# Kernel optimization log

Measured on AMD Instinct MI355X. Metric: run time of the kernel, lower is better.

## Reference

```python
import jax, jax.numpy as jnp
import numpy as np

EPS = 1e-5


def _conv(x, w, padding, groups=1):
    return jax.lax.conv_general_dilated(
        x, w, window_strides=(1, 1),
        padding=[(padding, padding), (padding, padding)],
        dimension_numbers=("NCHW", "OIHW", "NCHW"),
        feature_group_count=groups)


def _bn(x, gamma, beta, mean, var):
    # inference-mode BatchNorm2d, params shape [C]
    inv = gamma * jax.lax.rsqrt(var + EPS)
    return x * inv[None, :, None, None] + (beta - mean * inv)[None, :, None, None]


def _adder_dw(x, w):
    # depthwise AdderNet 'conv': out[b, c*R+r, h, w] = -sum_{kh,kw} |x[b,c,h+kh-p,w+kw-p] - w[c,r,kh,kw]|
    # x: [B,C,H,W], w: [C,R,K,K] (groups=C, R outputs per group)
    B, C, H, W = x.shape
    R, K = w.shape[1], w.shape[-1]
    p = K // 2
    xp = jnp.pad(x, ((0, 0), (0, 0), (p, p), (p, p)))
    acc = jnp.zeros((B, C, R, H, W), x.dtype)
    for kh in range(K):          # fixed small 3x3 tap loop
        for kw in range(K):
            shift = xp[:, :, kh:kh + H, kw:kw + W]          # [B,C,H,W]
            tap = w[:, :, kh, kw]                           # [C,R]
            acc = acc + jnp.abs(shift[:, :, None] - tap[None, :, :, None, None])
    return -acc.reshape(B, C * R, H, W)


def setup_inputs() -> dict:
    key = jax.random.key(0)
    ks = jax.random.split(key, 12)
    B, Cin, H, W = 32, 240, 56, 56
    init_c, ratio = 24, 10
    r1 = ratio - 1            # 9 ghost channels per primary channel
    new_c = init_c * r1       # 216
    f32 = jnp.float32
    x = jax.random.normal(ks[0], (B, Cin, H, W), f32)
    w_primary = jax.random.normal(ks[1], (init_c, Cin, 1, 1), f32) * 0.05
    w_dw = jax.random.normal(ks[2], (init_c, 1, 3, 3), f32) * 0.1
    w_add = jax.random.normal(ks[3], (init_c, r1, 3, 3), f32) * 0.1
    def bn(kk, c):
        k1, k2 = jax.random.split(kk)
        return (jnp.ones((c,), f32), jnp.zeros((c,), f32),
                jax.random.normal(k1, (c,), f32) * 0.1,
                jax.random.uniform(k2, (c,), f32, 0.5, 1.5))
    g1, b1, m1, v1 = bn(ks[4], init_c)
    g2, b2, m2, v2 = bn(ks[5], init_c)
    g3, b3, m3, v3 = bn(ks[6], new_c)
    return dict(x=x, w_primary=w_primary, g1=g1, b1=b1, m1=m1, v1=v1,
                w_dw=w_dw, g2=g2, b2=b2, m2=m2, v2=v2,
                w_add=w_add, g3=g3, b3=b3, m3=m3, v3=v3)


def reference(x, w_primary, g1, b1, m1, v1, w_dw, g2, b2, m2, v2,
              w_add, g3, b3, m3, v3):
    oup = 240
    init_c = w_primary.shape[0]
    # primary_conv: 1x1 conv -> BN -> depthwise 3x3 conv -> BN -> Identity (relu slot is Identity)
    x1 = _conv(x, w_primary, padding=0)
    x1 = _bn(x1, g1, b1, m1, v1)
    x1 = _conv(x1, w_dw, padding=1, groups=init_c)
    x1 = _bn(x1, g2, b2, m2, v2)
    # cheap_operation: depthwise Adder2D -> BN -> ReLU
    x2 = _adder_dw(x1, w_add)
    x2 = jax.nn.relu(_bn(x2, g3, b3, m3, v3))
    out = jnp.concatenate([x1, x2], axis=1)
    return out[:, :oup]
```

## Files before the change

### kernel.cpp

```cpp
#include <hip/hip_runtime.h>

#define EPS_ 1e-5f
#define BATCH 32
#define CIN 240
#define H_ 56
#define W_ 56
#define HW 3136
#define C1 24
#define R_ 9
#define C2 216
#define COUT 240

#define WS_WT   0
#define WS_B1   5760
#define WS_WDW  5784
#define WS_B2   6000
#define WS_INV3 6024
#define WS_T3   6240
#define WS_T1   8192
#define WS_T1_FLOATS (8192 + BATCH * C1 * HW)

__global__ __launch_bounds__(256) void prep_kernel(
    const float* __restrict__ wp,
    const float* __restrict__ g1, const float* __restrict__ b1,
    const float* __restrict__ m1, const float* __restrict__ v1,
    const float* __restrict__ wdw,
    const float* __restrict__ g2, const float* __restrict__ b2,
    const float* __restrict__ m2, const float* __restrict__ v2,
    const float* __restrict__ g3, const float* __restrict__ b3,
    const float* __restrict__ m3, const float* __restrict__ v3,
    float* __restrict__ ws) {
  int i = blockIdx.x * 256 + threadIdx.x;
  if (i < 5760) {
    int ci = i / C1, co = i % C1;
    float s = g1[co] / sqrtf(v1[co] + EPS_);
    ws[WS_WT + ci * C1 + co] = wp[co * CIN + ci] * s;
    if (ci == 0) ws[WS_B1 + co] = b1[co] - m1[co] * s;
  } else if (i < 5760 + C2) {
    int j = i - 5760;
    int c = j / 9;
    float s = g2[c] / sqrtf(v2[c] + EPS_);
    ws[WS_WDW + j] = wdw[j] * s;
    if (j % 9 == 0) ws[WS_B2 + c] = b2[c] - m2[c] * s;
  } else if (i < 5976 + C2) {
    int j = i - 5976;
    float s = g3[j] / sqrtf(v3[j] + EPS_);
    ws[WS_INV3 + j] = s;
    ws[WS_T3 + j] = b3[j] - m3[j] * s;
  }
}

__global__ __launch_bounds__(256) void conv1x1_kernel(
    const float* __restrict__ x, const float* __restrict__ wt,
    const float* __restrict__ bias1, float* __restrict__ t1b,
    const int cs, const int coff) {
  __shared__ float smem[12288];
  const int tid  = threadIdx.x;
  const int lane = tid & 63;
  const int kq   = tid >> 6;

  for (int i = tid; i < 5760; i += 256) smem[i] = wt[i];
  __syncthreads();

  const int P   = blockIdx.x * 128 + lane * 2;
  const int b   = P / HW;
  const int hw  = P - b * HW;
  const int ci0 = kq * 60;
  const float* xp    = x + ((size_t)b * CIN + ci0) * HW + hw;
  const float* wbase = smem + ci0 * C1;

  float acc[C1][2];
#pragma unroll
  for (int i = 0; i < C1; ++i) { acc[i][0] = 0.f; acc[i][1] = 0.f; }

  float2 A[6], B[6];
#pragma unroll
  for (int j = 0; j < 6; ++j) A[j] = *(const float2*)(xp + (size_t)j * HW);
#pragma unroll
  for (int j = 0; j < 6; ++j) B[j] = *(const float2*)(xp + (size_t)(6 + j) * HW);

  auto consume = [&](const float2* buf, int cb) {
#pragma unroll
    for (int j = 0; j < 6; ++j) {
      const float2 xv = buf[j];
      const float* wr = wbase + (cb + j) * C1;
#pragma unroll
      for (int k = 0; k < 6; ++k) {
        const float4 wq = *(const float4*)(wr + 4 * k);
        acc[4*k+0][0] = fmaf(wq.x, xv.x, acc[4*k+0][0]);
        acc[4*k+0][1] = fmaf(wq.x, xv.y, acc[4*k+0][1]);
        acc[4*k+1][0] = fmaf(wq.y, xv.x, acc[4*k+1][0]);
        acc[4*k+1][1] = fmaf(wq.y, xv.y, acc[4*k+1][1]);
        acc[4*k+2][0] = fmaf(wq.z, xv.x, acc[4*k+2][0]);
        acc[4*k+2][1] = fmaf(wq.z, xv.y, acc[4*k+2][1]);
        acc[4*k+3][0] = fmaf(wq.w, xv.x, acc[4*k+3][0]);
        acc[4*k+3][1] = fmaf(wq.w, xv.y, acc[4*k+3][1]);
      }
    }
  };

#pragma unroll 1
  for (int g = 0; g < 4; ++g) {
    const int c = 12 * g;
    consume(A, c);
#pragma unroll
    for (int j = 0; j < 6; ++j) A[j] = *(const float2*)(xp + (size_t)(c + 12 + j) * HW);
    consume(B, c + 6);
#pragma unroll
    for (int j = 0; j < 6; ++j) B[j] = *(const float2*)(xp + (size_t)(c + 18 + j) * HW);
  }
  consume(A, 48);
  consume(B, 54);
  __syncthreads();

#pragma unroll
  for (int i = 0; i < C1; ++i)
    *(float2*)&smem[(kq * C1 + i) * 128 + 2 * lane] = make_float2(acc[i][0], acc[i][1]);
  __syncthreads();

  float* o = t1b + ((size_t)b * cs + coff) * HW + hw;
#pragma unroll
  for (int i = 0; i < 6; ++i) {
    const int co = kq * 6 + i;
    const float2 p0 = *(const float2*)&smem[(0 * C1 + co) * 128 + 2 * lane];
    const float2 p1 = *(const float2*)&smem[(1 * C1 + co) * 128 + 2 * lane];
    const float2 p2 = *(const float2*)&smem[(2 * C1 + co) * 128 + 2 * lane];
    const float2 p3 = *(const float2*)&smem[(3 * C1 + co) * 128 + 2 * lane];
    const float bsv = bias1[co];
    float2 v;
    v.x = p0.x + p1.x + p2.x + p3.x + bsv;
    v.y = p0.y + p1.y + p2.y + p3.y + bsv;
    *(float2*)(o + (size_t)co * HW) = v;
  }
}

__global__ __launch_bounds__(256) void dwadd_kernel(
    const float* __restrict__ t1b, const float* __restrict__ wdwf,
    const float* __restrict__ bias2, const float* __restrict__ wadd,
    const float* __restrict__ inv3, const float* __restrict__ t3,
    float* __restrict__ out) {
  const int c = blockIdx.y, b = blockIdx.z;
  const int h0 = blockIdx.x * 14;
  __shared__ __align__(16) float t1s[18 * 56];
  __shared__ __align__(16) float x1s[16 * 56];
  __shared__ float taps[R_][3][4];
  __shared__ float s3[R_], t3s[R_];
  const int tid = threadIdx.x;

  const float* t1 = t1b + ((size_t)b * C1 + c) * HW;
  if (tid < 252) {
    const int r  = tid / 14;
    const int w0 = (tid - r * 14) * 4;
    const int gh = h0 - 2 + r;
    float4 v = {0.f, 0.f, 0.f, 0.f};
    if (gh >= 0 && gh < H_) v = *(const float4*)(t1 + gh * W_ + w0);
    *(float4*)&t1s[r * 56 + w0] = v;
  }
  if (tid < 108) {
    int r = tid / 12, kh = (tid / 4) % 3, kw = tid & 3;
    taps[r][kh][kw] = (kw < 3) ? wadd[((c * R_ + r) * 3 + kh) * 3 + kw] : 0.f;
  } else if (tid >= 128 && tid < 128 + R_) {
    int r = tid - 128;
    s3[r]  = inv3[c * R_ + r];
    t3s[r] = t3[c * R_ + r];
  }
  float wk[9];
#pragma unroll
  for (int k = 0; k < 9; ++k) wk[k] = wdwf[c * 9 + k];
  const float bb = bias2[c];
  __syncthreads();

  if (tid < 224) {
    const int r  = tid / 14;
    const int w0 = (tid - r * 14) * 4;
    const int gr = h0 - 1 + r;
    float4 v = {bb, bb, bb, bb};
#pragma unroll
    for (int kh = 0; kh < 3; ++kh) {
      const float* rp = &t1s[(r + kh) * 56];
      const float  l  = (w0 > 0) ? rp[w0 - 1] : 0.f;
      const float4 m  = *(const float4*)(rp + w0);
      const float  rt = (w0 < 52) ? rp[w0 + 4] : 0.f;
      const float t0 = wk[kh * 3 + 0], t1w = wk[kh * 3 + 1], t2 = wk[kh * 3 + 2];
      v.x = fmaf(l,   t0, v.x); v.x = fmaf(m.x, t1w, v.x); v.x = fmaf(m.y, t2, v.x);
      v.y = fmaf(m.x, t0, v.y); v.y = fmaf(m.y, t1w, v.y); v.y = fmaf(m.z, t2, v.y);
      v.z = fmaf(m.y, t0, v.z); v.z = fmaf(m.z, t1w, v.z); v.z = fmaf(m.w, t2, v.z);
      v.w = fmaf(m.z, t0, v.w); v.w = fmaf(m.w, t1w, v.w); v.w = fmaf(rt,  t2, v.w);
    }
    float4 xv = v;
    if (gr < 0 || gr >= H_) { xv.x = 0.f; xv.y = 0.f; xv.z = 0.f; xv.w = 0.f; }
    *(float4*)&x1s[r * 56 + w0] = xv;
    if (r >= 1 && r < 15)
      *(float4*)(out + ((size_t)b * COUT + c) * HW + gr * W_ + w0) = v;
  }
  __syncthreads();

  if (tid < 196) {
    const int r  = tid / 14;
    const int w0 = (tid - r * 14) * 4;
    const int gr = h0 + r;
    float xr[3][6];
#pragma unroll
    for (int kh = 0; kh < 3; ++kh) {
      const float* rp = &x1s[(r + kh) * 56];
      xr[kh][0] = (w0 > 0) ? rp[w0 - 1] : 0.f;
      const float4 m = *(const float4*)(rp + w0);
      xr[kh][1] = m.x; xr[kh][2] = m.y; xr[kh][3] = m.z; xr[kh][4] = m.w;
      xr[kh][5] = (w0 < 52) ? rp[w0 + 4] : 0.f;
    }
    float* ob = out + ((size_t)b * COUT + C1 + c * R_) * HW + gr * W_ + w0;
#pragma unroll
    for (int rr = 0; rr < R_; ++rr) {
      float a0 = 0.f, a1 = 0.f, a2 = 0.f, a3 = 0.f;
#pragma unroll
      for (int kh = 0; kh < 3; ++kh) {
#pragma unroll
        for (int kw = 0; kw < 3; ++kw) {
          const float t = taps[rr][kh][kw];
          a0 += fabsf(xr[kh][kw + 0] - t);
          a1 += fabsf(xr[kh][kw + 1] - t);
          a2 += fabsf(xr[kh][kw + 2] - t);
          a3 += fabsf(xr[kh][kw + 3] - t);
        }
      }
      const float s = s3[rr], tb = t3s[rr];
      float4 v;
      v.x = fmaxf(fmaf(-s, a0, tb), 0.f);
      v.y = fmaxf(fmaf(-s, a1, tb), 0.f);
      v.z = fmaxf(fmaf(-s, a2, tb), 0.f);
      v.w = fmaxf(fmaf(-s, a3, tb), 0.f);
      *(float4*)(ob + (size_t)rr * HW) = v;
    }
  }
}


__global__ __launch_bounds__(256) void dw_kernel(
    const float* __restrict__ outr, const float* __restrict__ wdwf,
    const float* __restrict__ bias2, float* __restrict__ out) {
  const int c = blockIdx.y, b = blockIdx.z;
  const int q = blockIdx.x * 256 + threadIdx.x;
  if (q >= 784) return;
  const int h  = q / 14;
  const int w0 = (q - h * 14) * 4;
  const float* in = outr + ((size_t)b * COUT + C1 + c) * HW;

  float wk[9];
#pragma unroll
  for (int k = 0; k < 9; ++k) wk[k] = wdwf[c * 9 + k];
  const float bb = bias2[c];

  float xr[3][6];
#pragma unroll
  for (int kh = 0; kh < 3; ++kh) {
    const int hh = h + kh - 1;
    const bool rok = (hh >= 0) & (hh < H_);
    const float* rp = in + hh * W_;
    xr[kh][0] = (rok && w0 > 0) ? rp[w0 - 1] : 0.f;
    if (rok) {
      const float4 m = *(const float4*)(rp + w0);
      xr[kh][1] = m.x; xr[kh][2] = m.y; xr[kh][3] = m.z; xr[kh][4] = m.w;
    } else {
      xr[kh][1] = 0.f; xr[kh][2] = 0.f; xr[kh][3] = 0.f; xr[kh][4] = 0.f;
    }
    xr[kh][5] = (rok && w0 < W_ - 4) ? rp[w0 + 4] : 0.f;
  }

  float4 v = {bb, bb, bb, bb};
#pragma unroll
  for (int kh = 0; kh < 3; ++kh) {
#pragma unroll
    for (int kw = 0; kw < 3; ++kw) {
      const float t = wk[kh * 3 + kw];
      v.x = fmaf(xr[kh][kw + 0], t, v.x);
      v.y = fmaf(xr[kh][kw + 1], t, v.y);
      v.z = fmaf(xr[kh][kw + 2], t, v.z);
      v.w = fmaf(xr[kh][kw + 3], t, v.w);
    }
  }
  *(float4*)(out + ((size_t)b * COUT + c) * HW + h * W_ + w0) = v;
}

__global__ __launch_bounds__(256) void adder_kernel(
    const float* __restrict__ outr, const float* __restrict__ wadd,
    const float* __restrict__ inv3, const float* __restrict__ t3,
    float* __restrict__ out) {
  const int c = blockIdx.y, b = blockIdx.z;
  __shared__ float taps[R_][3][4];
  __shared__ float s3[R_], t3s[R_];
  const int tid = threadIdx.x;
  if (tid < 108) {
    int r = tid / 12, kh = (tid / 4) % 3, kw = tid & 3;
    taps[r][kh][kw] = (kw < 3) ? wadd[((c * R_ + r) * 3 + kh) * 3 + kw] : 0.f;
  } else if (tid >= 128 && tid < 128 + R_) {
    int r = tid - 128;
    s3[r]  = inv3[c * R_ + r];
    t3s[r] = t3[c * R_ + r];
  }
  __syncthreads();

  const int q = blockIdx.x * 256 + tid;
  if (q >= 784) return;
  const int h  = q / 14;
  const int w0 = (q - h * 14) * 4;
  const float* in = outr + ((size_t)b * COUT + c) * HW;

  float xr[3][6];
#pragma unroll
  for (int kh = 0; kh < 3; ++kh) {
    const int hh = h + kh - 1;
    const bool rok = (hh >= 0) & (hh < H_);
    const float* rp = in + hh * W_;
    xr[kh][0] = (rok && w0 > 0) ? rp[w0 - 1] : 0.f;
    if (rok) {
      const float4 m = *(const float4*)(rp + w0);
      xr[kh][1] = m.x; xr[kh][2] = m.y; xr[kh][3] = m.z; xr[kh][4] = m.w;
    } else {
      xr[kh][1] = 0.f; xr[kh][2] = 0.f; xr[kh][3] = 0.f; xr[kh][4] = 0.f;
    }
    xr[kh][5] = (rok && w0 < W_ - 4) ? rp[w0 + 4] : 0.f;
  }

#pragma unroll
  for (int r = 0; r < R_; ++r) {
    float a0 = 0.f, a1 = 0.f, a2 = 0.f, a3 = 0.f;
#pragma unroll
    for (int kh = 0; kh < 3; ++kh) {
#pragma unroll
      for (int kw = 0; kw < 3; ++kw) {
        const float t = taps[r][kh][kw];
        a0 += fabsf(xr[kh][kw + 0] - t);
        a1 += fabsf(xr[kh][kw + 1] - t);
        a2 += fabsf(xr[kh][kw + 2] - t);
        a3 += fabsf(xr[kh][kw + 3] - t);
      }
    }
    const float s = s3[r], bb = t3s[r];
    float4 v;
    v.x = fmaxf(fmaf(-s, a0, bb), 0.f);
    v.y = fmaxf(fmaf(-s, a1, bb), 0.f);
    v.z = fmaxf(fmaf(-s, a2, bb), 0.f);
    v.w = fmaxf(fmaf(-s, a3, bb), 0.f);
    *(float4*)(out + ((size_t)b * COUT + C1 + c * R_ + r) * HW + h * W_ + w0) = v;
  }
}

extern "C" void kernel_launch(void* const* d_in, const int* in_sizes, int n_in,
                              void* d_out, int out_size, void* d_ws, size_t ws_size,
                              hipStream_t stream) {
  const float* x    = (const float*)d_in[0];
  const float* wp   = (const float*)d_in[1];
  const float* g1   = (const float*)d_in[2];
  const float* b1   = (const float*)d_in[3];
  const float* m1   = (const float*)d_in[4];
  const float* v1   = (const float*)d_in[5];
  const float* wdw  = (const float*)d_in[6];
  const float* g2   = (const float*)d_in[7];
  const float* b2   = (const float*)d_in[8];
  const float* m2   = (const float*)d_in[9];
  const float* v2   = (const float*)d_in[10];
  const float* wadd = (const float*)d_in[11];
  const float* g3   = (const float*)d_in[12];
  const float* b3   = (const float*)d_in[13];
  const float* m3   = (const float*)d_in[14];
  const float* v3   = (const float*)d_in[15];

  float* ws  = (float*)d_ws;
  float* out = (float*)d_out;

  const bool fused = ws_size >= (size_t)WS_T1_FLOATS * sizeof(float);
  float* t1b;
  int cs, coff;
  if (fused) { t1b = ws + WS_T1; cs = C1;   coff = 0; }
  else       { t1b = out;        cs = COUT; coff = C1; }

  prep_kernel<<<25, 256, 0, stream>>>(wp, g1, b1, m1, v1, wdw, g2, b2, m2, v2,
                                      g3, b3, m3, v3, ws);

  conv1x1_kernel<<<784, 256, 0, stream>>>(x, ws + WS_WT, ws + WS_B1,
                                          t1b, cs, coff);

  if (fused) {
    dwadd_kernel<<<dim3(4, C1, BATCH), 256, 0, stream>>>(
        t1b, ws + WS_WDW, ws + WS_B2, wadd, ws + WS_INV3, ws + WS_T3, out);
  } else {
    dw_kernel<<<dim3(4, C1, BATCH), 256, 0, stream>>>(out, ws + WS_WDW,
                                                      ws + WS_B2, out);
    adder_kernel<<<dim3(4, C1, BATCH), 256, 0, stream>>>(out, wadd,
                                                         ws + WS_INV3,
                                                         ws + WS_T3, out);
  }
}
```

Before: 219.1 us.

## Split conv1x1 output channels across 512 threads and read weights from global

The 1x1 conv kernel now launches 512 threads per block, with each wave group owning 12 of the 24 output channels for one quarter of the input channels. This halves the per-thread accumulator registers. Weights are read straight from global/L1 instead of being staged in LDS, which removes the preload loop and one barrier. The shared-memory reduction is reorganised to match, and an indexing fix offsets the adder kernel's input by C1 channels in the non-fused path.

```diff
diff --git a/kernel.cpp b/kernel.cpp
--- a/kernel.cpp
+++ b/kernel.cpp
@@ -50,28 +50,27 @@
   }
 }
 
-__global__ __launch_bounds__(256) void conv1x1_kernel(
+__global__ __launch_bounds__(512, 6) void conv1x1_kernel(
     const float* __restrict__ x, const float* __restrict__ wt,
     const float* __restrict__ bias1, float* __restrict__ t1b,
     const int cs, const int coff) {
-  __shared__ float smem[12288];
+  __shared__ float red[4 * C1 * 128];
   const int tid  = threadIdx.x;
   const int lane = tid & 63;
   const int kq   = tid >> 6;
-
-  for (int i = tid; i < 5760; i += 256) smem[i] = wt[i];
-  __syncthreads();
+  const int c4   = kq & 3;
+  const int co0  = (kq >> 2) * 12;
 
   const int P   = blockIdx.x * 128 + lane * 2;
   const int b   = P / HW;
   const int hw  = P - b * HW;
-  const int ci0 = kq * 60;
-  const float* xp    = x + ((size_t)b * CIN + ci0) * HW + hw;
-  const float* wbase = smem + ci0 * C1;
-
-  float acc[C1][2];
-#pragma unroll
-  for (int i = 0; i < C1; ++i) { acc[i][0] = 0.f; acc[i][1] = 0.f; }
+  const int ci0 = c4 * 60;
+  const float* xp = x  + ((size_t)b * CIN + ci0) * HW + hw;
+  const float* wb = wt + ci0 * C1 + co0;
+
+  float acc[12][2];
+#pragma unroll
+  for (int i = 0; i < 12; ++i) { acc[i][0] = 0.f; acc[i][1] = 0.f; }
 
   float2 A[6], B[6];
 #pragma unroll
@@ -83,9 +82,9 @@
 #pragma unroll
     for (int j = 0; j < 6; ++j) {
       const float2 xv = buf[j];
-      const float* wr = wbase + (cb + j) * C1;
-#pragma unroll
-      for (int k = 0; k < 6; ++k) {
+      const float* wr = wb + (cb + j) * C1;
+#pragma unroll
+      for (int k = 0; k < 3; ++k) {
         const float4 wq = *(const float4*)(wr + 4 * k);
         acc[4*k+0][0] = fmaf(wq.x, xv.x, acc[4*k+0][0]);
         acc[4*k+0][1] = fmaf(wq.x, xv.y, acc[4*k+0][1]);
@@ -111,21 +110,21 @@
   }
   consume(A, 48);
   consume(B, 54);
+
+#pragma unroll
+  for (int i = 0; i < 12; ++i)
+    *(float2*)&red[(c4 * C1 + co0 + i) * 128 + 2 * lane] =
+        make_float2(acc[i][0], acc[i][1]);
   __syncthreads();
 
-#pragma unroll
-  for (int i = 0; i < C1; ++i)
-    *(float2*)&smem[(kq * C1 + i) * 128 + 2 * lane] = make_float2(acc[i][0], acc[i][1]);
-  __syncthreads();
-
   float* o = t1b + ((size_t)b * cs + coff) * HW + hw;
 #pragma unroll
-  for (int i = 0; i < 6; ++i) {
-    const int co = kq * 6 + i;
-    const float2 p0 = *(const float2*)&smem[(0 * C1 + co) * 128 + 2 * lane];
-    const float2 p1 = *(const float2*)&smem[(1 * C1 + co) * 128 + 2 * lane];
-    const float2 p2 = *(const float2*)&smem[(2 * C1 + co) * 128 + 2 * lane];
-    const float2 p3 = *(const float2*)&smem[(3 * C1 + co) * 128 + 2 * lane];
+  for (int i = 0; i < 3; ++i) {
+    const int co = kq * 3 + i;
+    const float2 p0 = *(const float2*)&red[(0 * C1 + co) * 128 + 2 * lane];
+    const float2 p1 = *(const float2*)&red[(1 * C1 + co) * 128 + 2 * lane];
+    const float2 p2 = *(const float2*)&red[(2 * C1 + co) * 128 + 2 * lane];
+    const float2 p3 = *(const float2*)&red[(3 * C1 + co) * 128 + 2 * lane];
     const float bsv = bias1[co];
     float2 v;
     v.x = p0.x + p1.x + p2.x + p3.x + bsv;
@@ -303,7 +302,7 @@
   if (q >= 784) return;
   const int h  = q / 14;
   const int w0 = (q - h * 14) * 4;
-  const float* in = outr + ((size_t)b * COUT + c) * HW;
+  const float* in = outr + ((size_t)b * COUT + C1 + c) * HW;
 
   float xr[3][6];
 #pragma unroll
@@ -377,7 +376,7 @@
   prep_kernel<<<25, 256, 0, stream>>>(wp, g1, b1, m1, v1, wdw, g2, b2, m2, v2,
                                       g3, b3, m3, v3, ws);
 
-  conv1x1_kernel<<<784, 256, 0, stream>>>(x, ws + WS_WT, ws + WS_B1,
+  conv1x1_kernel<<<784, 512, 0, stream>>>(x, ws + WS_WT, ws + WS_B1,
                                           t1b, cs, coff);
 
   if (fused) {
```

Measured after the change: 297.9 us. 36.0% more time.

## Read 1x1 conv weights as wave-uniform scalar loads and use one pixel per thread

Applied to the files above, without the earlier changes.

The 1x1 conv kernel stops staging the weight matrix in LDS. It marks the weight pointer wave-uniform with readfirstlane so weights can be fetched through scalar loads. Each thread now handles one pixel instead of two, which doubles the grid to 1568 blocks and shrinks the LDS reduction buffer. The change also corrects the adder kernel's fallback input offset to read from channel C1+c. In exchange it relies on the compiler emitting scalar loads, and each weight load now feeds only one FMA instead of two.

```diff
diff --git a/kernel.cpp b/kernel.cpp
--- a/kernel.cpp
+++ b/kernel.cpp
@@ -50,52 +50,47 @@
   }
 }
 
+__device__ inline const float* uniform_ptr(const float* p) {
+  uint64_t u = (uint64_t)(uintptr_t)p;
+  uint32_t lo = __builtin_amdgcn_readfirstlane((uint32_t)(u & 0xffffffffu));
+  uint32_t hi = __builtin_amdgcn_readfirstlane((uint32_t)(u >> 32));
+  return (const float*)(uintptr_t)(((uint64_t)hi << 32) | lo);
+}
+
 __global__ __launch_bounds__(256) void conv1x1_kernel(
     const float* __restrict__ x, const float* __restrict__ wt,
     const float* __restrict__ bias1, float* __restrict__ t1b,
     const int cs, const int coff) {
-  __shared__ float smem[12288];
+  __shared__ float red[4 * C1 * 64];
   const int tid  = threadIdx.x;
   const int lane = tid & 63;
   const int kq   = tid >> 6;
 
-  for (int i = tid; i < 5760; i += 256) smem[i] = wt[i];
-  __syncthreads();
-
-  const int P   = blockIdx.x * 128 + lane * 2;
+  const int P   = blockIdx.x * 64 + lane;
   const int b   = P / HW;
   const int hw  = P - b * HW;
   const int ci0 = kq * 60;
-  const float* xp    = x + ((size_t)b * CIN + ci0) * HW + hw;
-  const float* wbase = smem + ci0 * C1;
-
-  float acc[C1][2];
-#pragma unroll
-  for (int i = 0; i < C1; ++i) { acc[i][0] = 0.f; acc[i][1] = 0.f; }
-
-  float2 A[6], B[6];
-#pragma unroll
-  for (int j = 0; j < 6; ++j) A[j] = *(const float2*)(xp + (size_t)j * HW);
-#pragma unroll
-  for (int j = 0; j < 6; ++j) B[j] = *(const float2*)(xp + (size_t)(6 + j) * HW);
-
-  auto consume = [&](const float2* buf, int cb) {
+  const float* xp = x + ((size_t)b * CIN + ci0) * HW + hw;
+  const float* wu = uniform_ptr(wt + ci0 * C1);
+
+  float acc[C1];
+#pragma unroll
+  for (int i = 0; i < C1; ++i) acc[i] = 0.f;
+
+  float A[6], B[6];
+#pragma unroll
+  for (int j = 0; j < 6; ++j) A[j] = xp[(size_t)j * HW];
+#pragma unroll
+  for (int j = 0; j < 6; ++j) B[j] = xp[(size_t)(6 + j) * HW];
+
+  auto consume = [&](const float* buf, int cb) {
 #pragma unroll
     for (int j = 0; j < 6; ++j) {
-      const float2 xv = buf[j];
-      const float* wr = wbase + (cb + j) * C1;
-#pragma unroll
-      for (int k = 0; k < 6; ++k) {
-        const float4 wq = *(const float4*)(wr + 4 * k);
-        acc[4*k+0][0] = fmaf(wq.x, xv.x, acc[4*k+0][0]);
-        acc[4*k+0][1] = fmaf(wq.x, xv.y, acc[4*k+0][1]);
-        acc[4*k+1][0] = fmaf(wq.y, xv.x, acc[4*k+1][0]);
-        acc[4*k+1][1] = fmaf(wq.y, xv.y, acc[4*k+1][1]);
-        acc[4*k+2][0] = fmaf(wq.z, xv.x, acc[4*k+2][0]);
-        acc[4*k+2][1] = fmaf(wq.z, xv.y, acc[4*k+2][1]);
-        acc[4*k+3][0] = fmaf(wq.w, xv.x, acc[4*k+3][0]);
-        acc[4*k+3][1] = fmaf(wq.w, xv.y, acc[4*k+3][1]);
-      }
+      const float xv = buf[j];
+      const float* wr = wu + (cb + j) * C1;
+#pragma unroll
+      for (int k = 0; k < C1; ++k)
+        acc[k] = fmaf(wr[k], xv, acc[k]);
     }
   };
 
@@ -104,33 +99,28 @@
     const int c = 12 * g;
     consume(A, c);
 #pragma unroll
-    for (int j = 0; j < 6; ++j) A[j] = *(const float2*)(xp + (size_t)(c + 12 + j) * HW);
+    for (int j = 0; j < 6; ++j) A[j] = xp[(size_t)(c + 12 + j) * HW];
     consume(B, c + 6);
 #pragma unroll
-    for (int j = 0; j < 6; ++j) B[j] = *(const float2*)(xp + (size_t)(c + 18 + j) * HW);
+    for (int j = 0; j < 6; ++j) B[j] = xp[(size_t)(c + 18 + j) * HW];
   }
   consume(A, 48);
   consume(B, 54);
-  __syncthreads();
-
-#pragma unroll
-  for (int i = 0; i < C1; ++i)
-    *(float2*)&smem[(kq * C1 + i) * 128 + 2 * lane] = make_float2(acc[i][0], acc[i][1]);
+
+#pragma unroll
+  for (int i = 0; i < C1; ++i) red[(kq * C1 + i) * 64 + lane] = acc[i];
   __syncthreads();
 
   float* o = t1b + ((size_t)b * cs + coff) * HW + hw;
 #pragma unroll
   for (int i = 0; i < 6; ++i) {
     const int co = kq * 6 + i;
-    const float2 p0 = *(const float2*)&smem[(0 * C1 + co) * 128 + 2 * lane];
-    const float2 p1 = *(const float2*)&smem[(1 * C1 + co) * 128 + 2 * lane];
-    const float2 p2 = *(const float2*)&smem[(2 * C1 + co) * 128 + 2 * lane];
-    const float2 p3 = *(const float2*)&smem[(3 * C1 + co) * 128 + 2 * lane];
-    const float bsv = bias1[co];
-    float2 v;
-    v.x = p0.x + p1.x + p2.x + p3.x + bsv;
-    v.y = p0.y + p1.y + p2.y + p3.y + bsv;
-    *(float2*)(o + (size_t)co * HW) = v;
+    float v = red[(0 * C1 + co) * 64 + lane]
+            + red[(1 * C1 + co) * 64 + lane]
+            + red[(2 * C1 + co) * 64 + lane]
+            + red[(3 * C1 + co) * 64 + lane]
+            + bias1[co];
+    o[(size_t)co * HW] = v;
   }
 }
 
@@ -303,7 +293,7 @@
   if (q >= 784) return;
   const int h  = q / 14;
   const int w0 = (q - h * 14) * 4;
-  const float* in = outr + ((size_t)b * COUT + c) * HW;
+  const float* in = outr + ((size_t)b * COUT + C1 + c) * HW;
 
   float xr[3][6];
 #pragma unroll
@@ -377,8 +367,8 @@
   prep_kernel<<<25, 256, 0, stream>>>(wp, g1, b1, m1, v1, wdw, g2, b2, m2, v2,
                                       g3, b3, m3, v3, ws);
 
-  conv1x1_kernel<<<784, 256, 0, stream>>>(x, ws + WS_WT, ws + WS_B1,
-                                          t1b, cs, coff);
+  conv1x1_kernel<<<1568, 256, 0, stream>>>(x, ws + WS_WT, ws + WS_B1,
+                                           t1b, cs, coff);
 
   if (fused) {
     dwadd_kernel<<<dim3(4, C1, BATCH), 256, 0, stream>>>(
```

New measurement: 274.7 us. 25.4% more time.
